# Performance work log

Hardware: AMD Instinct MI355X
Metric: run time of the kernel (lower is better)

## Reference

```python
import jax, jax.numpy as jnp
import numpy as np

BS, NV, D, DFF, E, H = 32, 512, 128, 512, 8, 8
EPS = 1e-5

def layernorm(x, g, b):
    m = x.mean(-1, keepdims=True)
    v = ((x - m) ** 2).mean(-1, keepdims=True)
    return (x - m) / jnp.sqrt(v + EPS) * g + b

def setup_inputs() -> dict:
    key = jax.random.key(0)
    ks = jax.random.split(key, 10)
    s = lambda k, shape: (jax.random.normal(k, shape, jnp.float32) * 0.02)
    return {
        "x": jax.random.normal(ks[0], (BS, NV, D), jnp.float32),
        "cls_emd": jax.random.normal(ks[1], (E, D), jnp.float32),
        "Wq": s(ks[2], (D, D)), "Wk": s(ks[3], (D, D)),
        "Wv": s(ks[4], (D, D)), "Wo": s(ks[5], (D, D)),
        "Wg": s(ks[6], (D, D)),
        "W1": s(ks[7], (E, DFF, 2 * D)), "b1": jnp.zeros((E, DFF), jnp.float32),
        "W2": s(ks[8], (E, D, DFF)), "b2": jnp.zeros((E, D), jnp.float32),
        "g1": jnp.ones((D,), jnp.float32), "be1": jnp.zeros((D,), jnp.float32),
        "g2": jnp.ones((D,), jnp.float32), "be2": jnp.zeros((D,), jnp.float32),
    }

def reference(x, cls_emd, Wq, Wk, Wv, Wo, Wg, W1, b1, W2, b2, g1, be1, g2, be2):
    bs, n, d = x.shape
    dh = d // H
    # --- full multi-head self-attention over the variate axis ---
    q = (x @ Wq).reshape(bs, n, H, dh)
    k = (x @ Wk).reshape(bs, n, H, dh)
    v = (x @ Wv).reshape(bs, n, H, dh)
    scores = jnp.einsum('bnhd,bmhd->bhnm', q, k) * (1.0 / np.sqrt(dh))
    attn = jax.nn.softmax(scores, axis=-1)            # [bs, H, n, n]
    new_x = jnp.einsum('bhnm,bmhd->bnhd', attn, v).reshape(bs, n, d) @ Wo
    # residual + norm1 (dropout = identity in eval)
    x = layernorm(x + new_x, g1, be1)
    # --- gating: per-variate scores over clusters [n_vars, n_clusters] ---
    gate_scores = jax.nn.softmax((x.mean(0) @ Wg) @ cls_emd.T, axis=-1)
    # --- MoE: expand tokens vs every cluster, concat, per-cluster expert MLP ---
    ncl = cls_emd.shape[0]
    y = jnp.broadcast_to(x[:, :, None, :], (bs, n, ncl, d))
    z = jnp.broadcast_to(cls_emd[None, None, :, :], (bs, n, ncl, d))
    yz_cat = jnp.concatenate([y, z], axis=-1)          # [bs, n, K, 2d]
    h = jax.nn.relu(jnp.einsum('bnkc,kfc->bnkf', yz_cat, W1) + b1)  # kernel_size=1 conv == matmul
    expert_out = jnp.einsum('bnkf,kdf->bnkd', h, W2) + b2           # [bs, n, K, d]
    y_r = jnp.einsum('nk,bnkd->bnd', gate_scores, expert_out)
    out = layernorm(x + y_r, g2, be2)
    return (out, attn, gate_scores)
```

## Files before the change

kernel.cpp:

```cpp
#include <hip/hip_runtime.h>
#include <hip/hip_bf16.h>
#include <math.h>

#define BS   32
#define NV   512
#define D    128
#define DFF  512
#define E    8
#define NH   8
#define DH   16
#define M_TOK (BS*NV)
#define EPS  1e-5f

typedef __hip_bfloat16 bf16;
typedef _Float16 f16;
using sh8   = __attribute__((ext_vector_type(8))) short;
using h4    = __attribute__((ext_vector_type(4))) _Float16;
using h8    = __attribute__((ext_vector_type(8))) _Float16;
using f32x4 = __attribute__((ext_vector_type(4))) float;

__device__ __forceinline__ float b2f(bf16 v){ return __bfloat162float(v); }
__device__ __forceinline__ bf16  f2b(float v){ return __float2bfloat16(v); }

__device__ __forceinline__ void gload_lds16(const void* g, void* l){
    __builtin_amdgcn_global_load_lds(
        (const __attribute__((address_space(1))) unsigned int*)g,
        (__attribute__((address_space(3))) unsigned int*)l, 16, 0, 0);
}

__global__ __launch_bounds__(256) void k_f2b(
    const float* __restrict__ in, bf16* __restrict__ out, int n)
{
    int i = blockIdx.x*256 + threadIdx.x;
    if (i < n) out[i] = f2b(in[i]);
}

__global__ __launch_bounds__(256) void k_xh(
    const float* __restrict__ in, f16* __restrict__ outp, int n)
{
    int i = (blockIdx.x*256 + threadIdx.x)*4;
    if (i < n){
        float4 vv = *(const float4*)(in+i);
        h4 o; o[0]=(f16)vv.x; o[1]=(f16)vv.y; o[2]=(f16)vv.z; o[3]=(f16)vv.w;
        *(h4*)(outp+i) = o;
    }
}

__global__ __launch_bounds__(256) void k_wtqkv(
    const float* __restrict__ Wq, const float* __restrict__ Wk, const float* __restrict__ Wv,
    f16* __restrict__ WT)
{
    int idx = blockIdx.x*256 + threadIdx.x;
    int c = idx>>7, kk = idx&127;
    int which = c>>7, col = c&127;
    const float* W = which==0?Wq:(which==1?Wk:Wv);
    WT[idx] = (f16)W[kk*D + col];
}

__global__ __launch_bounds__(256) void k_wto(
    const float* __restrict__ Wo, f16* __restrict__ WoT)
{
    int idx = blockIdx.x*256 + threadIdx.x;
    int c = idx>>7, kk = idx&127;
    WoT[idx] = (f16)Wo[kk*D + c];
}

__global__ __launch_bounds__(512) void k_qkv_mfma(
    const f16* __restrict__ xh, const f16* __restrict__ WT,
    f16* __restrict__ q, f16* __restrict__ k, f16* __restrict__ v)
{
    __shared__ __align__(16) char smem[65536];
    char* Xl = smem;
    char* Wl = smem + 16384;
    int t = threadIdx.x;
    int w = t>>6, lane = t&63;
    int bm = blockIdx.x, nh = blockIdx.y;

    const f16* xsrc = xh + (size_t)bm*64*D;
    #pragma unroll
    for (int i=0;i<2;++i){
        int ci = i*512 + t;
        int row = ci>>4, c16 = (ci&15)^(row&7);
        gload_lds16(xsrc + row*D + c16*8, Xl + (size_t)(i*512 + w*64)*16);
    }
    const f16* wsrc = WT + (size_t)nh*192*D;
    #pragma unroll
    for (int i=0;i<6;++i){
        int ci = i*512 + t;
        int row = ci>>4, c16 = (ci&15)^(row&7);
        gload_lds16(wsrc + row*D + c16*8, Wl + (size_t)(i*512 + w*64)*16);
    }
    __syncthreads();

    int rblk = w>>1, ch = w&1;
    int rl = lane&15, g = lane>>4;

    h8 afr[4];
    #pragma unroll
    for (int kk=0;kk<4;++kk){
        int row = rblk*16 + rl;
        int bo = (row<<8) + (kk<<6) + (g<<4); bo ^= (row&7)<<4;
        afr[kk] = *(const h8*)(Xl + bo);
    }
    f32x4 acc[6];
    #pragma unroll
    for (int nt=0;nt<6;++nt) acc[nt] = (f32x4){0.f,0.f,0.f,0.f};
    #pragma unroll
    for (int nt=0; nt<6; ++nt){
        #pragma unroll
        for (int kk=0;kk<4;++kk){
            int row = ch*96 + nt*16 + rl;
            int bo = (row<<8)+(kk<<6)+(g<<4); bo ^= (row&7)<<4;
            h8 bfr = *(const h8*)(Wl + bo);
            acc[nt] = __builtin_amdgcn_mfma_f32_16x16x32_f16(afr[kk], bfr, acc[nt],0,0,0);
        }
    }
    #pragma unroll
    for (int nt=0;nt<6;++nt){
        int cidx = nh*192 + ch*96 + nt*16 + rl;
        int which = cidx>>7, hh=(cidx>>4)&7, d = cidx&15;
        f16* dst = which==0?q:(which==1?k:v);
        #pragma unroll
        for (int j=0;j<4;++j){
            int m = bm*64 + rblk*16 + g*4 + j;
            int b = m>>9, n = m&511;
            dst[(((size_t)(b*NH+hh))*NV + n)*DH + d] = (f16)acc[nt][j];
        }
    }
}

#define KSTRIDE 24
#define VSTRIDE 520
__global__ __launch_bounds__(256) void k_attn2(
    const f16* __restrict__ q, const f16* __restrict__ kin, const f16* __restrict__ vin,
    float* __restrict__ attn_out, f16* __restrict__ ctx)
{
    __shared__ f16  Kl[512*KSTRIDE];
    __shared__ f16  VT[16*VSTRIDE];
    __shared__ f16  pbh[4][16*36];

    int bh = blockIdx.x;
    int t  = threadIdx.x;
    const f16* kb = kin + (size_t)bh*NV*DH;
    const f16* vb = vin + (size_t)bh*NV*DH;

    {
        int r0 = t*2;
        #pragma unroll
        for (int rr=0; rr<2; ++rr){
            const uint4* src = (const uint4*)(kb + (size_t)(r0+rr)*DH);
            *((uint4*)(Kl + (r0+rr)*KSTRIDE))     = src[0];
            *((uint4*)(Kl + (r0+rr)*KSTRIDE + 8)) = src[1];
        }
        const unsigned short* v0s = (const unsigned short*)(vb + (size_t)r0*DH);
        const unsigned short* v1s = v0s + DH;
        #pragma unroll
        for (int d=0; d<DH; ++d){
            unsigned u = (unsigned)v0s[d] | ((unsigned)v1s[d] << 16);
            *((unsigned*)(VT + d*VSTRIDE + r0)) = u;
        }
    }
    __syncthreads();

    int wave = t >> 6, lane = t & 63;
    int ql = lane & 15, g = lane >> 4;
    int q0 = blockIdx.y*64 + wave*16;

    h4 qf = *(const h4*)(q + ((size_t)bh*NV + q0 + ql)*DH + 4*g);
    #pragma unroll
    for (int i=0;i<4;++i) qf[i] = qf[i] * (_Float16)0.36067376f;

    f32x4 S[32];
    #pragma unroll
    for (int tt=0; tt<32; ++tt){
        h4 kf = *(const h4*)(Kl + (tt*16 + ql)*KSTRIDE + 4*g);
        S[tt] = __builtin_amdgcn_mfma_f32_16x16x16f16(kf, qf, (f32x4){0.f,0.f,0.f,0.f}, 0,0,0);
    }

    float sum = 0.f;
    #pragma unroll
    for (int tt=0; tt<32; ++tt)
        #pragma unroll
        for (int j=0;j<4;++j){
            float p = exp2f(S[tt][j]);
            S[tt][j] = p; sum += p;
        }
    sum += __shfl_xor(sum, 16);
    sum += __shfl_xor(sum, 32);
    float inv = 1.f/sum;
    #pragma unroll
    for (int tt=0; tt<32; ++tt)
        #pragma unroll
        for (int j=0;j<4;++j) S[tt][j] *= inv;

    f32x4 o0 = (f32x4){0.f,0.f,0.f,0.f}, o1 = (f32x4){0.f,0.f,0.f,0.f};
    f16* pw = pbh[wave];
    float* attnbase = attn_out + ((size_t)bh*NV + q0)*NV;
    int kvq = (lane&7)*4, qh = lane>>3;
    #pragma unroll
    for (int c=0; c<16; ++c){
        #pragma unroll
        for (int tt2=0; tt2<2; ++tt2){
            int tt = c*2 + tt2;
            h4 pf;
            pf[0]=(f16)S[tt][0]; pf[1]=(f16)S[tt][1];
            pf[2]=(f16)S[tt][2]; pf[3]=(f16)S[tt][3];
            h4 vf = *(const h4*)(VT + ql*VSTRIDE + tt*16 + 4*g);
            if (tt2) o1 = __builtin_amdgcn_mfma_f32_16x16x16f16(vf, pf, o1, 0,0,0);
            else     o0 = __builtin_amdgcn_mfma_f32_16x16x16f16(vf, pf, o0, 0,0,0);
            *(h4*)(pw + ql*36 + tt2*16 + 4*g) = pf;
        }
        asm volatile("" ::: "memory");
        #pragma unroll
        for (int r=0;r<2;++r){
            int qq = r*8 + qh;
            h4 hv = *(const h4*)(pw + qq*36 + kvq);
            f32x4 vv;
            vv[0]=(float)hv[0]; vv[1]=(float)hv[1];
            vv[2]=(float)hv[2]; vv[3]=(float)hv[3];
            __builtin_nontemporal_store(vv, (f32x4*)(attnbase + (size_t)qq*NV + c*32 + kvq));
        }
        asm volatile("" ::: "memory");
    }
    f32x4 o = o0 + o1;
    int b = bh >> 3, h = bh & 7;
    f16* cb = ctx + ((size_t)(b*NV) + q0 + ql)*D + h*DH + 4*g;
    #pragma unroll
    for (int j=0;j<4;++j) cb[j] = (f16)o[j];
}

__global__ __launch_bounds__(512) void k_woln_mfma(
    const f16* __restrict__ ctx, const f16* __restrict__ WoT,
    const float* __restrict__ x, const float* __restrict__ g1, const float* __restrict__ be1,
    bf16* __restrict__ x1b, float* __restrict__ yacc)
{
    __shared__ __align__(16) char smem[49152];
    __shared__ float lnred[2][64][2];
    char* Cl = smem;
    char* Wl = smem + 16384;
    int t = threadIdx.x;
    int w = t>>6, lane = t&63;
    int bm = blockIdx.x;

    const f16* csrc = ctx + (size_t)bm*64*D;
    #pragma unroll
    for (int i=0;i<2;++i){
        int ci = i*512 + t;
        int row = ci>>4, c16 = (ci&15)^(row&7);
        gload_lds16(csrc + row*D + c16*8, Cl + (size_t)(i*512 + w*64)*16);
    }
    #pragma unroll
    for (int i=0;i<4;++i){
        int ci = i*512 + t;
        int row = ci>>4, c16 = (ci&15)^(row&7);
        gload_lds16(WoT + row*D + c16*8, Wl + (size_t)(i*512 + w*64)*16);
    }
    __syncthreads();

    int rblk = w>>1, ch = w&1;
    int rl = lane&15, g = lane>>4;

    h8 afr[4];
    #pragma unroll
    for (int kk=0;kk<4;++kk){
        int row = rblk*16 + rl;
        int bo = (row<<8) + (kk<<6) + (g<<4); bo ^= (row&7)<<4;
        afr[kk] = *(const h8*)(Cl + bo);
    }
    f32x4 acc[4];
    #pragma unroll
    for (int nt=0;nt<4;++nt) acc[nt] = (f32x4){0.f,0.f,0.f,0.f};
    #pragma unroll
    for (int nt=0; nt<4; ++nt){
        #pragma unroll
        for (int kk=0;kk<4;++kk){
            int row = ch*64 + nt*16 + rl;
            int bo = (row<<8)+(kk<<6)+(g<<4); bo ^= (row&7)<<4;
            h8 bfr = *(const h8*)(Wl + bo);
            acc[nt] = __builtin_amdgcn_mfma_f32_16x16x32_f16(afr[kk], bfr, acc[nt],0,0,0);
        }
    }

    float rowv[4][4];
    #pragma unroll
    for (int j=0;j<4;++j){
        int m = bm*64 + rblk*16 + g*4 + j;
        #pragma unroll
        for (int dt=0;dt<4;++dt){
            int d = ch*64 + dt*16 + rl;
            rowv[j][dt] = acc[dt][j] + x[(size_t)m*D + d];
        }
    }
    #pragma unroll
    for (int j=0;j<4;++j){
        float s  = rowv[j][0]+rowv[j][1]+rowv[j][2]+rowv[j][3];
        float s2 = rowv[j][0]*rowv[j][0]+rowv[j][1]*rowv[j][1]
                 + rowv[j][2]*rowv[j][2]+rowv[j][3]*rowv[j][3];
        #pragma unroll
        for (int o=1;o<16;o<<=1){ s += __shfl_xor(s,o); s2 += __shfl_xor(s2,o); }
        if (rl==0){
            int row = rblk*16 + g*4 + j;
            lnred[ch][row][0] = s;
            lnred[ch][row][1] = s2;
        }
    }
    __syncthreads();
    #pragma unroll
    for (int j=0;j<4;++j){
        int row = rblk*16 + g*4 + j;
        float S  = lnred[0][row][0] + lnred[1][row][0];
        float S2 = lnred[0][row][1] + lnred[1][row][1];
        float mean = S*(1.f/D);
        float var  = S2*(1.f/D) - mean*mean;
        float rs = rsqrtf(var + EPS);
        int m = bm*64 + row;
        #pragma unroll
        for (int dt=0;dt<4;++dt){
            int d = ch*64 + dt*16 + rl;
            float o1 = (rowv[j][dt]-mean)*rs*g1[d] + be1[d];
            x1b[(size_t)m*D + d] = f2b(o1);
            yacc[(size_t)m*D + d] = o1;
        }
    }
}

__global__ __launch_bounds__(128) void k_gate(
    const float* __restrict__ yacc, const float* __restrict__ Wg, const float* __restrict__ cls,
    float* __restrict__ gate, float* __restrict__ gate_out)
{
    __shared__ float xm[D];
    __shared__ float tt[D];
    __shared__ float se[E];
    int n = blockIdx.x, t = threadIdx.x;
    float s = 0.f;
    #pragma unroll
    for (int b=0;b<BS;++b) s += yacc[((size_t)b*NV + n)*D + t];
    xm[t] = s * (1.f/BS);
    __syncthreads();
    float a = 0.f;
    for (int c=0;c<D;++c) a += xm[c] * Wg[c*D + t];
    tt[t] = a;
    __syncthreads();
    if (t < E){
        float acc=0.f;
        for (int c=0;c<D;++c) acc += tt[c] * cls[t*D + c];
        se[t]=acc;
    }
    __syncthreads();
    if (t==0){
        float mx=se[0];
        for(int e=1;e<E;++e) mx=fmaxf(mx,se[e]);
        float sm=0.f; float p[E];
        for(int e=0;e<E;++e){ p[e]=__expf(se[e]-mx); sm+=p[e]; }
        float inv=1.f/sm;
        for(int e=0;e<E;++e){
            gate[n*E+e]     = p[e]*inv;
            gate_out[n*E+e] = p[e]*inv;
        }
    }
}

__global__ __launch_bounds__(256) void k_b1eff(
    const float* __restrict__ W1, const float* __restrict__ b1, const float* __restrict__ cls,
    float* __restrict__ b1eff)
{
    int idx = blockIdx.x*256 + threadIdx.x;
    int e = idx >> 9, f = idx & 511;
    float acc = b1[e*DFF + f];
    const float* wrow = W1 + ((size_t)e*DFF + f)*(2*D) + D;
    #pragma unroll 8
    for (int c=0;c<D;++c) acc += cls[e*D+c] * wrow[c];
    b1eff[e*DFF+f]=acc;
}

__global__ __launch_bounds__(512) void k_moe_fused(
    const bf16* __restrict__ x1b, const bf16* __restrict__ W1b, const bf16* __restrict__ W2b,
    const float* __restrict__ b1eff, const float* __restrict__ b2,
    const float* __restrict__ gate, const float* __restrict__ yacc,
    const float* __restrict__ g2, const float* __restrict__ be2,
    float* __restrict__ out)
{
    __shared__ __align__(16) char smem[147456];
    char* Hl = smem + 131072;
    float (*lnred)[64][2] = (float (*)[64][2])Hl;

    int t = threadIdx.x;
    int w = t >> 6, lane = t & 63;
    int rblk = w >> 1, c = w & 1;
    int rl = lane & 15, g = lane >> 4;
    int bm = blockIdx.x;

    sh8 afr[4];
    {
        const bf16* Ab = x1b + (size_t)(bm*64 + rblk*16 + rl)*D;
        #pragma unroll
        for (int kk=0;kk<4;++kk) afr[kk] = *(const sh8*)(Ab + kk*32 + g*8);
    }

    f32x4 oacc[4];
    #pragma unroll
    for (int dt=0;dt<4;++dt) oacc[dt] = (f32x4){0.f,0.f,0.f,0.f};

    auto STAGE = [&](int idx, int buf){
        int e = idx >> 2, fc = idx & 3;
        const bf16* w1src = W1b + ((size_t)e*DFF + fc*128)*(2*D);
        const bf16* w2src = W2b + (size_t)e*D*DFF + fc*128;
        char* Wa = smem + buf*65536;
        char* Wb = Wa + 32768;
        #pragma unroll
        for (int i=0;i<4;++i){
            int ci  = (i*8 + w)*64 + lane;
            int row = ci >> 4;
            int c16 = (ci & 15) ^ (row & 7);
            gload_lds16(w1src + (size_t)row*256 + c16*8, Wa + (size_t)(i*8+w)*1024);
            gload_lds16(w2src + (size_t)row*512 + c16*8, Wb + (size_t)(i*8+w)*1024);
        }
    };

    STAGE(0, 0);
    asm volatile("s_waitcnt vmcnt(0)" ::: "memory");
    __syncthreads();

    f32x4 acc2e[4];
    #pragma unroll
    for (int dt=0;dt<4;++dt) acc2e[dt] = (f32x4){0.f,0.f,0.f,0.f};

    for (int idx=0; idx<32; ++idx){
        int buf = idx & 1;
        int e = idx >> 2, fc = idx & 3;
        char* Wa = smem + buf*65536;
        char* Wb = Wa + 32768;

        if (idx < 31) STAGE(idx+1, buf^1);

        f32x4 acc1[4];
        #pragma unroll
        for (int ft=0;ft<4;++ft) acc1[ft] = (f32x4){0.f,0.f,0.f,0.f};
        #pragma unroll
        for (int ft=0; ft<4; ++ft){
            int row = c*64 + ft*16 + rl;
            #pragma unroll
            for (int kk=0;kk<4;++kk){
                int bo = (row<<8) + (kk<<6) + (g<<4);
                bo ^= (row&7)<<4;
                sh8 bfr = *(const sh8*)(Wa + bo);
                acc1[ft] = __builtin_amdgcn_mfma_f32_16x16x32_bf16(afr[kk], bfr, acc1[ft], 0,0,0);
            }
        }
        #pragma unroll
        for (int ft=0; ft<4; ++ft){
            int fl = c*64 + ft*16 + rl;
            float bia = b1eff[e*DFF + fc*128 + fl];
            #pragma unroll
            for (int j=0;j<4;++j){
                int row = rblk*16 + g*4 + j;
                float v = acc1[ft][j] + bia;
                v = v > 0.f ? v : 0.f;
                int bo = (row<<8) + (fl<<1);
                bo ^= (row&7)<<4;
                *(bf16*)(Hl + bo) = f2b(v);
            }
        }
        __syncthreads();

        #pragma unroll
        for (int kk=0; kk<4; ++kk){
            int rowH = rblk*16 + rl;
            int boH = (rowH<<8) + (kk<<6) + (g<<4);
            boH ^= (rowH&7)<<4;
            sh8 hfr = *(const sh8*)(Hl + boH);
            #pragma unroll
            for (int dt=0;dt<4;++dt){
                int rowW = c*64 + dt*16 + rl;
                int boW = (rowW<<8) + (kk<<6) + (g<<4);
                boW ^= (rowW&7)<<4;
                sh8 bfr = *(const sh8*)(Wb + boW);
                acc2e[dt] = __builtin_amdgcn_mfma_f32_16x16x32_bf16(hfr, bfr, acc2e[dt], 0,0,0);
            }
        }

        if (fc == 3){
            #pragma unroll
            for (int j=0;j<4;++j){
                int m  = bm*64 + rblk*16 + g*4 + j;
                float gv = gate[(m & 511)*E + e];
                #pragma unroll
                for (int dt=0;dt<4;++dt){
                    int d = c*64 + dt*16 + rl;
                    oacc[dt][j] += gv*(acc2e[dt][j] + b2[e*D + d]);
                }
            }
            #pragma unroll
            for (int dt=0;dt<4;++dt) acc2e[dt] = (f32x4){0.f,0.f,0.f,0.f};
        }

        asm volatile("s_waitcnt vmcnt(0)" ::: "memory");
        __syncthreads();
    }

    float rowv[4][4];
    #pragma unroll
    for (int j=0;j<4;++j){
        int m = bm*64 + rblk*16 + g*4 + j;
        #pragma unroll
        for (int dt=0;dt<4;++dt){
            int d = c*64 + dt*16 + rl;
            rowv[j][dt] = oacc[dt][j] + yacc[(size_t)m*D + d];
        }
    }
    #pragma unroll
    for (int j=0;j<4;++j){
        float s  = rowv[j][0]+rowv[j][1]+rowv[j][2]+rowv[j][3];
        float s2 = rowv[j][0]*rowv[j][0]+rowv[j][1]*rowv[j][1]
                 + rowv[j][2]*rowv[j][2]+rowv[j][3]*rowv[j][3];
        #pragma unroll
        for (int o=1;o<16;o<<=1){ s += __shfl_xor(s,o); s2 += __shfl_xor(s2,o); }
        if (rl==0){
            int row = rblk*16 + g*4 + j;
            lnred[c][row][0] = s;
            lnred[c][row][1] = s2;
        }
    }
    __syncthreads();
    #pragma unroll
    for (int j=0;j<4;++j){
        int row = rblk*16 + g*4 + j;
        float S  = lnred[0][row][0] + lnred[1][row][0];
        float S2 = lnred[0][row][1] + lnred[1][row][1];
        float mean = S*(1.f/D);
        float var  = S2*(1.f/D) - mean*mean;
        float rs = rsqrtf(var + EPS);
        int m = bm*64 + row;
        #pragma unroll
        for (int dt=0;dt<4;++dt){
            int d = c*64 + dt*16 + rl;
            out[(size_t)m*D + d] = (rowv[j][dt]-mean)*rs*g2[d] + be2[d];
        }
    }
}

extern "C" void kernel_launch(void* const* d_in, const int* in_sizes, int n_in,
                              void* d_out, int out_size, void* d_ws, size_t ws_size,
                              hipStream_t stream)
{
    const float* x   = (const float*)d_in[0];
    const float* cls = (const float*)d_in[1];
    const float* Wq  = (const float*)d_in[2];
    const float* Wk  = (const float*)d_in[3];
    const float* Wv  = (const float*)d_in[4];
    const float* Wo  = (const float*)d_in[5];
    const float* Wg  = (const float*)d_in[6];
    const float* W1  = (const float*)d_in[7];
    const float* b1  = (const float*)d_in[8];
    const float* W2  = (const float*)d_in[9];
    const float* b2  = (const float*)d_in[10];
    const float* g1  = (const float*)d_in[11];
    const float* be1 = (const float*)d_in[12];
    const float* g2  = (const float*)d_in[13];
    const float* be2 = (const float*)d_in[14];

    float* out      = (float*)d_out;
    float* attn     = out + (size_t)M_TOK*D;
    float* gate_out = attn + (size_t)BS*NH*NV*NV;

    char* ws = (char*)d_ws;
    size_t off = 0;
    auto alloc = [&](size_t bytes)->void*{ void* p = ws + off; off += (bytes + 255) & ~(size_t)255; return p; };
    f16*   q    = (f16*)  alloc((size_t)M_TOK*D*2);
    f16*   kbuf = (f16*)  alloc((size_t)M_TOK*D*2);
    f16*   vbuf = (f16*)  alloc((size_t)M_TOK*D*2);
    f16*   ctx  = (f16*)  alloc((size_t)M_TOK*D*2);
    bf16*  x1b  = (bf16*) alloc((size_t)M_TOK*D*2);
    float* yacc = (float*)alloc((size_t)M_TOK*D*4);
    float* gate = (float*)alloc((size_t)NV*E*4);
    float* b1eff= (float*)alloc((size_t)E*DFF*4);
    bf16*  W1b  = (bf16*) alloc((size_t)E*DFF*2*D*2);
    bf16*  W2b  = (bf16*) alloc((size_t)E*D*DFF*2);
    f16*   xh   = (f16*)  alloc((size_t)M_TOK*D*2);
    f16*   WTq  = (f16*)  alloc((size_t)384*D*2);
    f16*   WoT  = (f16*)  alloc((size_t)D*D*2);

    const int nW1 = E*DFF*2*D;
    const int nW2 = E*D*DFF;
    const int nX  = M_TOK*D;
    k_f2b<<<(nW1+255)/256, 256, 0, stream>>>(W1, W1b, nW1);
    k_f2b<<<(nW2+255)/256, 256, 0, stream>>>(W2, W2b, nW2);
    k_xh <<<(nX/4+255)/256, 256, 0, stream>>>(x, xh, nX);
    k_wtqkv<<<192, 256, 0, stream>>>(Wq, Wk, Wv, WTq);
    k_wto  <<<64, 256, 0, stream>>>(Wo, WoT);

    k_qkv_mfma<<<dim3(M_TOK/64, 2), 512, 0, stream>>>(xh, WTq, q, kbuf, vbuf);
    k_attn2<<<dim3(BS*NH, NV/64), 256, 0, stream>>>(q, kbuf, vbuf, attn, ctx);
    k_woln_mfma<<<M_TOK/64, 512, 0, stream>>>(ctx, WoT, x, g1, be1, x1b, yacc);
    k_gate<<<NV, 128, 0, stream>>>(yacc, Wg, cls, gate, gate_out);
    k_b1eff<<<(E*DFF)/256, 256, 0, stream>>>(W1, b1, cls, b1eff);
    k_moe_fused<<<256, 512, 0, stream>>>(x1b, W1b, W2b, b1eff, b2, gate, yacc, g2, be2, out);
}
```

Baseline: 179.2 us.

## Merge weight/input prep kernels into one launch and store attn probabilities directly

```diff
diff --git a/kernel.cpp b/kernel.cpp
--- a/kernel.cpp
+++ b/kernel.cpp
@@ -15,12 +15,17 @@
 typedef __hip_bfloat16 bf16;
 typedef _Float16 f16;
 using sh8   = __attribute__((ext_vector_type(8))) short;
+using us4   = __attribute__((ext_vector_type(4))) unsigned short;
 using h4    = __attribute__((ext_vector_type(4))) _Float16;
 using h8    = __attribute__((ext_vector_type(8))) _Float16;
 using f32x4 = __attribute__((ext_vector_type(4))) float;
 
 __device__ __forceinline__ float b2f(bf16 v){ return __bfloat162float(v); }
 __device__ __forceinline__ bf16  f2b(float v){ return __float2bfloat16(v); }
+__device__ __forceinline__ unsigned short f2bu(float v){
+    bf16 b = __float2bfloat16(v);
+    return __builtin_bit_cast(unsigned short, b);
+}
 
 __device__ __forceinline__ void gload_lds16(const void* g, void* l){
     __builtin_amdgcn_global_load_lds(
@@ -28,41 +33,56 @@
         (__attribute__((address_space(3))) unsigned int*)l, 16, 0, 0);
 }
 
-__global__ __launch_bounds__(256) void k_f2b(
-    const float* __restrict__ in, bf16* __restrict__ out, int n)
-{
-    int i = blockIdx.x*256 + threadIdx.x;
-    if (i < n) out[i] = f2b(in[i]);
-}
-
-__global__ __launch_bounds__(256) void k_xh(
-    const float* __restrict__ in, f16* __restrict__ outp, int n)
-{
-    int i = (blockIdx.x*256 + threadIdx.x)*4;
-    if (i < n){
-        float4 vv = *(const float4*)(in+i);
+#define PR0 4096
+#define PR1 (PR0 + 262144)
+#define PR2 (PR1 + 131072)
+#define PR3 (PR2 + 524288)
+#define PR4 (PR3 + 49152)
+#define PR5 (PR4 + 16384)
+#define PREP_ITEMS PR5
+__global__ __launch_bounds__(256) void k_prep(
+    const float* __restrict__ W1, const float* __restrict__ W2,
+    const float* __restrict__ x,  const float* __restrict__ Wq,
+    const float* __restrict__ Wk, const float* __restrict__ Wv,
+    const float* __restrict__ Wo, const float* __restrict__ b1,
+    const float* __restrict__ cls,
+    bf16* __restrict__ W1b, bf16* __restrict__ W2b, f16* __restrict__ xh,
+    f16* __restrict__ WTq, f16* __restrict__ WoT, float* __restrict__ b1eff)
+{
+    int tid = blockIdx.x*256 + threadIdx.x;
+    if (tid < PR0){
+        int e = tid >> 9, f = tid & 511;
+        float acc = b1[e*DFF + f];
+        const float* wrow = W1 + ((size_t)e*DFF + f)*(2*D) + D;
+        #pragma unroll 8
+        for (int c=0;c<D;++c) acc += cls[e*D+c] * wrow[c];
+        b1eff[tid] = acc;
+    } else if (tid < PR1){
+        int i = (tid - PR0)*4;
+        float4 vv = *(const float4*)(W1 + i);
+        us4 o; o[0]=f2bu(vv.x); o[1]=f2bu(vv.y); o[2]=f2bu(vv.z); o[3]=f2bu(vv.w);
+        *(us4*)(W1b + i) = o;
+    } else if (tid < PR2){
+        int i = (tid - PR1)*4;
+        float4 vv = *(const float4*)(W2 + i);
+        us4 o; o[0]=f2bu(vv.x); o[1]=f2bu(vv.y); o[2]=f2bu(vv.z); o[3]=f2bu(vv.w);
+        *(us4*)(W2b + i) = o;
+    } else if (tid < PR3){
+        int i = (tid - PR2)*4;
+        float4 vv = *(const float4*)(x + i);
         h4 o; o[0]=(f16)vv.x; o[1]=(f16)vv.y; o[2]=(f16)vv.z; o[3]=(f16)vv.w;
-        *(h4*)(outp+i) = o;
-    }
-}
-
-__global__ __launch_bounds__(256) void k_wtqkv(
-    const float* __restrict__ Wq, const float* __restrict__ Wk, const float* __restrict__ Wv,
-    f16* __restrict__ WT)
-{
-    int idx = blockIdx.x*256 + threadIdx.x;
-    int c = idx>>7, kk = idx&127;
-    int which = c>>7, col = c&127;
-    const float* W = which==0?Wq:(which==1?Wk:Wv);
-    WT[idx] = (f16)W[kk*D + col];
-}
-
-__global__ __launch_bounds__(256) void k_wto(
-    const float* __restrict__ Wo, f16* __restrict__ WoT)
-{
-    int idx = blockIdx.x*256 + threadIdx.x;
-    int c = idx>>7, kk = idx&127;
-    WoT[idx] = (f16)Wo[kk*D + c];
+        *(h4*)(xh + i) = o;
+    } else if (tid < PR4){
+        int idx = tid - PR3;
+        int c = idx>>7, kk = idx&127;
+        int which = c>>7, col = c&127;
+        const float* W = which==0?Wq:(which==1?Wk:Wv);
+        WTq[idx] = (f16)W[kk*D + col];
+    } else if (tid < PR5){
+        int idx = tid - PR4;
+        int c = idx>>7, kk = idx&127;
+        WoT[idx] = (f16)Wo[kk*D + c];
+    }
 }
 
 __global__ __launch_bounds__(512) void k_qkv_mfma(
@@ -137,7 +157,6 @@
 {
     __shared__ f16  Kl[512*KSTRIDE];
     __shared__ f16  VT[16*VSTRIDE];
-    __shared__ f16  pbh[4][16*36];
 
     int bh = blockIdx.x;
     int t  = threadIdx.x;
@@ -194,33 +213,16 @@
         for (int j=0;j<4;++j) S[tt][j] *= inv;
 
     f32x4 o0 = (f32x4){0.f,0.f,0.f,0.f}, o1 = (f32x4){0.f,0.f,0.f,0.f};
-    f16* pw = pbh[wave];
-    float* attnbase = attn_out + ((size_t)bh*NV + q0)*NV;
-    int kvq = (lane&7)*4, qh = lane>>3;
-    #pragma unroll
-    for (int c=0; c<16; ++c){
-        #pragma unroll
-        for (int tt2=0; tt2<2; ++tt2){
-            int tt = c*2 + tt2;
-            h4 pf;
-            pf[0]=(f16)S[tt][0]; pf[1]=(f16)S[tt][1];
-            pf[2]=(f16)S[tt][2]; pf[3]=(f16)S[tt][3];
-            h4 vf = *(const h4*)(VT + ql*VSTRIDE + tt*16 + 4*g);
-            if (tt2) o1 = __builtin_amdgcn_mfma_f32_16x16x16f16(vf, pf, o1, 0,0,0);
-            else     o0 = __builtin_amdgcn_mfma_f32_16x16x16f16(vf, pf, o0, 0,0,0);
-            *(h4*)(pw + ql*36 + tt2*16 + 4*g) = pf;
-        }
-        asm volatile("" ::: "memory");
-        #pragma unroll
-        for (int r=0;r<2;++r){
-            int qq = r*8 + qh;
-            h4 hv = *(const h4*)(pw + qq*36 + kvq);
-            f32x4 vv;
-            vv[0]=(float)hv[0]; vv[1]=(float)hv[1];
-            vv[2]=(float)hv[2]; vv[3]=(float)hv[3];
-            __builtin_nontemporal_store(vv, (f32x4*)(attnbase + (size_t)qq*NV + c*32 + kvq));
-        }
-        asm volatile("" ::: "memory");
+    float* prow = attn_out + ((size_t)bh*NV + q0 + ql)*NV + 4*g;
+    #pragma unroll
+    for (int tt=0; tt<32; ++tt){
+        h4 pf;
+        pf[0]=(f16)S[tt][0]; pf[1]=(f16)S[tt][1];
+        pf[2]=(f16)S[tt][2]; pf[3]=(f16)S[tt][3];
+        h4 vf = *(const h4*)(VT + ql*VSTRIDE + tt*16 + 4*g);
+        if (tt&1) o1 = __builtin_amdgcn_mfma_f32_16x16x16f16(vf, pf, o1, 0,0,0);
+        else      o0 = __builtin_amdgcn_mfma_f32_16x16x16f16(vf, pf, o0, 0,0,0);
+        __builtin_nontemporal_store(S[tt], (f32x4*)(prow + tt*16));
     }
     f32x4 o = o0 + o1;
     int b = bh >> 3, h = bh & 7;
@@ -358,19 +360,6 @@
             gate_out[n*E+e] = p[e]*inv;
         }
     }
-}
-
-__global__ __launch_bounds__(256) void k_b1eff(
-    const float* __restrict__ W1, const float* __restrict__ b1, const float* __restrict__ cls,
-    float* __restrict__ b1eff)
-{
-    int idx = blockIdx.x*256 + threadIdx.x;
-    int e = idx >> 9, f = idx & 511;
-    float acc = b1[e*DFF + f];
-    const float* wrow = W1 + ((size_t)e*DFF + f)*(2*D) + D;
-    #pragma unroll 8
-    for (int c=0;c<D;++c) acc += cls[e*D+c] * wrow[c];
-    b1eff[e*DFF+f]=acc;
 }
 
 __global__ __launch_bounds__(512) void k_moe_fused(
@@ -580,19 +569,13 @@
     f16*   WTq  = (f16*)  alloc((size_t)384*D*2);
     f16*   WoT  = (f16*)  alloc((size_t)D*D*2);
 
-    const int nW1 = E*DFF*2*D;
-    const int nW2 = E*D*DFF;
-    const int nX  = M_TOK*D;
-    k_f2b<<<(nW1+255)/256, 256, 0, stream>>>(W1, W1b, nW1);
-    k_f2b<<<(nW2+255)/256, 256, 0, stream>>>(W2, W2b, nW2);
-    k_xh <<<(nX/4+255)/256, 256, 0, stream>>>(x, xh, nX);
-    k_wtqkv<<<192, 256, 0, stream>>>(Wq, Wk, Wv, WTq);
-    k_wto  <<<64, 256, 0, stream>>>(Wo, WoT);
+    k_prep<<<(PREP_ITEMS+255)/256, 256, 0, stream>>>(
+        W1, W2, x, Wq, Wk, Wv, Wo, b1, cls,
+        W1b, W2b, xh, WTq, WoT, b1eff);
 
     k_qkv_mfma<<<dim3(M_TOK/64, 2), 512, 0, stream>>>(xh, WTq, q, kbuf, vbuf);
     k_attn2<<<dim3(BS*NH, NV/64), 256, 0, stream>>>(q, kbuf, vbuf, attn, ctx);
     k_woln_mfma<<<M_TOK/64, 512, 0, stream>>>(ctx, WoT, x, g1, be1, x1b, yacc);
     k_gate<<<NV, 128, 0, stream>>>(yacc, Wg, cls, gate, gate_out);
-    k_b1eff<<<(E*DFF)/256, 256, 0, stream>>>(W1, b1, cls, b1eff);
     k_moe_fused<<<256, 512, 0, stream>>>(x1b, W1b, W2b, b1eff, b2, gate, yacc, g2, be2, out);
 }
```

After: 181.7 us. About the same (+1.4%).
